# Optimization experiments

Hardware: AMD Instinct MI355X
Metric: run time of the kernel (lower is better)

Reference implementation:

```python
import jax, jax.numpy as jnp
import numpy as np

# Norse LIFParameters defaults (method='super', alpha=100)
DT = 1e-3
TAU_SYN_INV = 200.0   # 1 / 5e-3
TAU_MEM_INV = 100.0   # 1 / 1e-2
V_TH = 1.0
V_LEAK = 0.0
V_RESET = 0.0
ALPHA = 100.0

@jax.custom_vjp
def superspike(x):
    return (x > 0).astype(x.dtype)

def _ss_fwd(x):
    return superspike(x), x

def _ss_bwd(x, g):
    return (g / (ALPHA * jnp.abs(x) + 1.0) ** 2,)

superspike.defvjp(_ss_fwd, _ss_bwd)

T, B, F, H1, OUT = 100, 512, 784, 1024, 10

def setup_inputs() -> dict:
    key = jax.random.key(0)
    k1, k2, k3 = jax.random.split(key, 3)
    x = jax.random.normal(k1, (T, B, F), jnp.float32)
    # fc0: Linear(784, h1) with bias
    W0 = jax.random.normal(k2, (H1, F), jnp.float32) / np.sqrt(F)
    b0 = jnp.zeros((H1,), jnp.float32)
    # LILinearCell input_weights: Linear(h1, 10) without bias
    Wout = jax.random.normal(k3, (OUT, H1), jnp.float32) / np.sqrt(H1)
    return {"x": x, "W0": W0, "b0": b0, "Wout": Wout}

def reference(x, W0, b0, Wout):
    Tn, Bn, Fn = x.shape
    H = W0.shape[0]
    O = Wout.shape[0]

    def step(state, xt):
        v_lif, i_lif, v_li, i_li = state
        z_in = xt @ W0.T + b0                                    # [B, H]
        # LIF cell step
        v_dec = v_lif + DT * TAU_MEM_INV * ((V_LEAK - v_lif) + i_lif)
        i_dec = i_lif * (1.0 - DT * TAU_SYN_INV)
        z = superspike(v_dec - V_TH)                             # spikes [B, H]
        v_new = (1.0 - z) * v_dec + z * V_RESET
        i_new = i_dec + z_in
        # LI linear cell step (voltage output)
        v_li_new = v_li + DT * TAU_MEM_INV * ((V_LEAK - v_li) + i_li)
        i_li_new = i_li * (1.0 - DT * TAU_SYN_INV) + z @ Wout.T  # [B, O]
        return (v_new, i_new, v_li_new, i_li_new), v_li_new

    z0 = lambda s: jnp.zeros(s, x.dtype)
    init = (z0((Bn, H)), z0((Bn, H)), z0((Bn, O)), z0((Bn, O)))
    _, voltages = jax.lax.scan(step, init, x)
    return voltages  # [T, B, 10]
```

## Files before the change

kernel.cpp:

```cpp
#include <hip/hip_runtime.h>

#define T_TOT 100
#define BATCH 512
#define FIN   784
#define HID   1024
#define NOUT  10
#define KP    800
#define BK    32
#define KSTEPS 25
#define NGRP  16

typedef _Float16 f16x8 __attribute__((ext_vector_type(8)));
typedef float    f32x4 __attribute__((ext_vector_type(4)));

#define AS1C(p) ((const __attribute__((address_space(1))) void*)(p))
#define AS3(p)  ((__attribute__((address_space(3))) void*)(p))

__global__ __launch_bounds__(256)
void cvt_split(const float* __restrict__ src, _Float16* __restrict__ hi,
               _Float16* __restrict__ lo, int nrows)
{
    int idx = blockIdx.x * 256 + threadIdx.x;
    if (idx >= nrows * 100) return;
    int row = idx / 100;
    int k0  = (idx - row * 100) * 8;
    f16x8 h, l;
    if (k0 < FIN) {
        float4 a = *(const float4*)(src + (size_t)row * FIN + k0);
        float4 b = *(const float4*)(src + (size_t)row * FIN + k0 + 4);
        float xs[8] = {a.x, a.y, a.z, a.w, b.x, b.y, b.z, b.w};
        #pragma unroll
        for (int j = 0; j < 8; ++j) {
            _Float16 hh = (_Float16)xs[j];
            h[j] = hh;
            l[j] = (_Float16)((xs[j] - (float)hh) * 4096.0f);
        }
    } else {
        #pragma unroll
        for (int j = 0; j < 8; ++j) { h[j] = (_Float16)0.f; l[j] = (_Float16)0.f; }
    }
    *(f16x8*)(hi + (size_t)row * KP + k0) = h;
    *(f16x8*)(lo + (size_t)row * KP + k0) = l;
}

__global__ __launch_bounds__(256, 2)
void gemm_mfma(const _Float16* __restrict__ Xhi, const _Float16* __restrict__ Xlo,
               const _Float16* __restrict__ Whi, const _Float16* __restrict__ Wlo,
               const float* __restrict__ bias, float* __restrict__ Z, int mb)
{
    __shared__ char smem[65536];
    const int tid  = threadIdx.x;
    const int lane = tid & 63;
    const int wid  = tid >> 6;
    const int wm   = wid >> 1;
    const int wn   = wid & 1;
    const int fr   = lane & 15;
    const int fg   = lane >> 4;

    const int j = blockIdx.x;
    int bm, bn;
    if ((mb & 7) == 0) {
        bm = (j & 7) | ((j >> 6) << 3);
        bn = (j >> 3) & 7;
    } else {
        bm = j >> 3;
        bn = j & 7;
    }
    const size_t row0 = (size_t)bm * 128;
    const int    col0 = bn * 128;

    f32x4 accm[4][4], accc[4][4];
    #pragma unroll
    for (int a = 0; a < 4; ++a)
        #pragma unroll
        for (int b = 0; b < 4; ++b) {
            accm[a][b] = (f32x4){0.f, 0.f, 0.f, 0.f};
            accc[a][b] = (f32x4){0.f, 0.f, 0.f, 0.f};
        }

    auto stage = [&](int buf, int kt) {
        const int kof = kt * BK;
        #pragma unroll
        for (int q = 0; q < 2; ++q) {
            const int lin = q * 256 + tid;
            const int row = lin >> 2;
            const int pos = lin & 3;
            const int gg  = pos ^ ((row >> 1) & 3);
            const int ldsw = buf * 32768 + q * 4096 + wid * 1024;
            const size_t ga = (row0 + row) * (size_t)KP + kof + gg * 8;
            const size_t gb = (size_t)(col0 + row) * KP + kof + gg * 8;
            __builtin_amdgcn_global_load_lds(AS1C(Xhi + ga), AS3(smem + ldsw),         16, 0, 0);
            __builtin_amdgcn_global_load_lds(AS1C(Xlo + ga), AS3(smem + ldsw +  8192), 16, 0, 0);
            __builtin_amdgcn_global_load_lds(AS1C(Whi + gb), AS3(smem + ldsw + 16384), 16, 0, 0);
            __builtin_amdgcn_global_load_lds(AS1C(Wlo + gb), AS3(smem + ldsw + 24576), 16, 0, 0);
        }
    };

    auto compute = [&](int buf) {
        const char* base = smem + buf * 32768;
        f16x8 ah[4], al[4], bh[4], bl[4];
        #pragma unroll
        for (int mf = 0; mf < 4; ++mf) {
            const int row = wm * 64 + mf * 16 + fr;
            const int off = row * 64 + ((fg ^ ((row >> 1) & 3)) << 4);
            ah[mf] = *(const f16x8*)(base + off);
            al[mf] = *(const f16x8*)(base + 8192 + off);
        }
        #pragma unroll
        for (int nf = 0; nf < 4; ++nf) {
            const int row = wn * 64 + nf * 16 + fr;
            const int off = row * 64 + ((fg ^ ((row >> 1) & 3)) << 4);
            bh[nf] = *(const f16x8*)(base + 16384 + off);
            bl[nf] = *(const f16x8*)(base + 24576 + off);
        }
        #pragma unroll
        for (int mf = 0; mf < 4; ++mf)
            #pragma unroll
            for (int nf = 0; nf < 4; ++nf) {
                accm[mf][nf] = __builtin_amdgcn_mfma_f32_16x16x32_f16(ah[mf], bh[nf], accm[mf][nf], 0, 0, 0);
                accc[mf][nf] = __builtin_amdgcn_mfma_f32_16x16x32_f16(ah[mf], bl[nf], accc[mf][nf], 0, 0, 0);
                accc[mf][nf] = __builtin_amdgcn_mfma_f32_16x16x32_f16(al[mf], bh[nf], accc[mf][nf], 0, 0, 0);
            }
    };

    stage(0, 0);
    int buf = 0;
    for (int kt = 0; kt < KSTEPS; ++kt) {
        __syncthreads();
        if (kt + 1 < KSTEPS) stage(buf ^ 1, kt + 1);
        compute(buf);
        buf ^= 1;
    }

    #pragma unroll
    for (int nf = 0; nf < 4; ++nf) {
        const int colg = col0 + wn * 64 + nf * 16 + fr;
        const float bv = bias[colg];
        #pragma unroll
        for (int mf = 0; mf < 4; ++mf) {
            const size_t rowg = row0 + wm * 64 + mf * 16 + fg * 4;
            #pragma unroll
            for (int i = 0; i < 4; ++i)
                Z[(rowg + i) * HID + colg] =
                    accm[mf][nf][i] + accc[mf][nf][i] * 2.44140625e-4f + bv;
        }
    }
}

__device__ __forceinline__ float dpp_sum16(float v)
{
    int x;
    x = __builtin_amdgcn_update_dpp(0, __builtin_bit_cast(int, v), 0xB1, 0xF, 0xF, true);
    v += __builtin_bit_cast(float, x);
    x = __builtin_amdgcn_update_dpp(0, __builtin_bit_cast(int, v), 0x4E, 0xF, 0xF, true);
    v += __builtin_bit_cast(float, x);
    x = __builtin_amdgcn_update_dpp(0, __builtin_bit_cast(int, v), 0x141, 0xF, 0xF, true);
    v += __builtin_bit_cast(float, x);
    x = __builtin_amdgcn_update_dpp(0, __builtin_bit_cast(int, v), 0x140, 0xF, 0xF, true);
    v += __builtin_bit_cast(float, x);
    return v;
}

__global__ __launch_bounds__(256, 2)
void lif_scan(const float* __restrict__ Z, const float* __restrict__ Wout,
              float* __restrict__ S,
              float* __restrict__ st_v, float* __restrict__ st_i,
              int tn, int first, int last)
{
#pragma clang fp contract(off)
    const int tid   = threadIdx.x;
    const int b     = blockIdx.x;
    const int lane  = tid & 63;
    const int w     = tid >> 6;
    const int hglob = w * 256 + lane * 4;

    float wreg[NOUT][4];
    #pragma unroll
    for (int o = 0; o < NOUT; ++o) {
        float4 t4 = *(const float4*)&Wout[o * HID + hglob];
        wreg[o][0] = t4.x; wreg[o][1] = t4.y; wreg[o][2] = t4.z; wreg[o][3] = t4.w;
    }

    float v[4], cu[4];
    if (first) {
        #pragma unroll
        for (int jj = 0; jj < 4; ++jj) { v[jj] = 0.f; cu[jj] = 0.f; }
    } else {
        float4 tv = *(const float4*)&st_v[(size_t)b * HID + hglob];
        float4 ti = *(const float4*)&st_i[(size_t)b * HID + hglob];
        v[0]=tv.x; v[1]=tv.y; v[2]=tv.z; v[3]=tv.w;
        cu[0]=ti.x; cu[1]=ti.y; cu[2]=ti.z; cu[3]=ti.w;
    }

    const float* Zb = Z + (size_t)b * HID + hglob;
    float4 z0 = *(const float4*)Zb;
    float4 z1 = (tn > 1) ? *(const float4*)(Zb + (size_t)BATCH * HID)     : z0;
    float4 z2 = (tn > 2) ? *(const float4*)(Zb + (size_t)2 * BATCH * HID) : z1;

    const int g = w * 4 + (lane >> 4);

    for (int t = 0; t < tn; ++t) {
        float4 zc = z0; z0 = z1; z1 = z2;
        if (t + 3 < tn) z2 = *(const float4*)(Zb + (size_t)(t + 3) * BATCH * HID);

        const float za[4] = {zc.x, zc.y, zc.z, zc.w};
        float zf[4];
        bool anyz = false;
        #pragma unroll
        for (int jj = 0; jj < 4; ++jj) {
            float tmp  = (0.0f - v[jj]) + cu[jj];
            float vdec = v[jj] + 0.1f * tmp;
            bool  z    = vdec > 1.0f;
            zf[jj] = z ? 1.0f : 0.0f;
            anyz   = anyz || z;
            v[jj]  = z ? 0.0f : vdec;
            cu[jj] = cu[jj] * 0.8f + za[jj];
        }

        float p[NOUT];
        #pragma unroll
        for (int o = 0; o < NOUT; ++o) p[o] = 0.f;

        if (__any(anyz)) {
            if (anyz) {
                #pragma unroll
                for (int o = 0; o < NOUT; ++o)
                    p[o] = zf[0]*wreg[o][0] + zf[1]*wreg[o][1]
                         + zf[2]*wreg[o][2] + zf[3]*wreg[o][3];
            }
            #pragma unroll
            for (int o = 0; o < NOUT; ++o) p[o] = dpp_sum16(p[o]);
        }

        if ((lane & 15) == 0) {
            float* sp = S + ((size_t)t * BATCH + b) * (NGRP * NOUT) + g * NOUT;
            #pragma unroll
            for (int o = 0; o < NOUT; ++o) sp[o] = p[o];
        }
    }

    if (!last) {
        *(float4*)&st_v[(size_t)b * HID + hglob] = make_float4(v[0], v[1], v[2], v[3]);
        *(float4*)&st_i[(size_t)b * HID + hglob] = make_float4(cu[0], cu[1], cu[2], cu[3]);
    }
}

__global__ __launch_bounds__(256)
void li_scan(const float* __restrict__ S, float* __restrict__ out,
             float* __restrict__ st_vli, float* __restrict__ st_ili,
             int t0, int tn, int first, int last)
{
#pragma clang fp contract(off)
    const int id = blockIdx.x * 256 + threadIdx.x;
    if (id >= BATCH * NOUT) return;
    const int b = id / NOUT;
    const int o = id - b * NOUT;

    float vli = 0.f, ili = 0.f;
    if (!first) { vli = st_vli[id]; ili = st_ili[id]; }

    const float* Sp = S + (size_t)b * (NGRP * NOUT) + o;
    for (int t = 0; t < tn; ++t) {
        const float* p = Sp + (size_t)t * BATCH * (NGRP * NOUT);
        float s = 0.f;
        #pragma unroll
        for (int gg = 0; gg < NGRP; ++gg) s += p[gg * NOUT];
        float tmp  = (0.0f - vli) + ili;
        float vnew = vli + 0.1f * tmp;
        ili = ili * 0.8f + s;
        vli = vnew;
        out[((size_t)(t0 + t) * BATCH + b) * NOUT + o] = vnew;
    }
    if (!last) { st_vli[id] = vli; st_ili[id] = ili; }
}

extern "C" void kernel_launch(void* const* d_in, const int* in_sizes, int n_in,
                              void* d_out, int out_size, void* d_ws, size_t ws_size,
                              hipStream_t stream)
{
    const float* x    = (const float*)d_in[0];
    const float* W0   = (const float*)d_in[1];
    const float* b0   = (const float*)d_in[2];
    const float* Wout = (const float*)d_in[3];
    float* out = (float*)d_out;

    char* ws = (char*)d_ws;
    float* st_v   = (float*)ws;
    float* st_i   = st_v   + (size_t)BATCH * HID;
    float* st_vli = st_i   + (size_t)BATCH * HID;
    float* st_ili = st_vli + BATCH * NOUT;
    _Float16* Whi = (_Float16*)(st_ili + BATCH * NOUT);
    _Float16* Wlo = Whi + (size_t)HID * KP;
    char* dyn = (char*)(Wlo + (size_t)HID * KP);

    const size_t fixed = (size_t)(dyn - ws);
    const size_t per_t = (size_t)BATCH * HID * 4
                       + (size_t)BATCH * KP * 2 * 2
                       + (size_t)BATCH * NGRP * NOUT * 4;
    size_t avail = (ws_size > fixed) ? ws_size - fixed : 0;
    int tch = (int)(avail / per_t);
    if (tch > T_TOT) tch = T_TOT;
    if (tch >= 2) tch &= ~1;
    if (tch < 1) tch = 1;

    float*    Zbuf = (float*)dyn;
    _Float16* Xhi  = (_Float16*)(dyn + (size_t)tch * BATCH * HID * 4);
    _Float16* Xlo  = Xhi + (size_t)tch * BATCH * KP;
    float*    Sbuf = (float*)(Xlo + (size_t)tch * BATCH * KP);

    hipLaunchKernelGGL(cvt_split, dim3((HID * 100 + 255) / 256), dim3(256), 0, stream,
                       W0, Whi, Wlo, HID);

    for (int t0 = 0; t0 < T_TOT; t0 += tch) {
        const int tn    = (T_TOT - t0 < tch) ? (T_TOT - t0) : tch;
        const int nrows = tn * BATCH;
        const int mb    = nrows / 128;

        hipLaunchKernelGGL(cvt_split, dim3((nrows * 100 + 255) / 256), dim3(256), 0, stream,
                           x + (size_t)t0 * BATCH * FIN, Xhi, Xlo, nrows);
        hipLaunchKernelGGL(gemm_mfma, dim3(mb * 8), dim3(256), 0, stream,
                           Xhi, Xlo, Whi, Wlo, b0, Zbuf, mb);
        hipLaunchKernelGGL(lif_scan, dim3(BATCH), dim3(256), 0, stream,
                           Zbuf, Wout, Sbuf, st_v, st_i,
                           tn, (t0 == 0) ? 1 : 0, (t0 + tn >= T_TOT) ? 1 : 0);
        hipLaunchKernelGGL(li_scan, dim3((BATCH * NOUT + 255) / 256), dim3(256), 0, stream,
                           Sbuf, out, st_vli, st_ili,
                           t0, tn, (t0 == 0) ? 1 : 0, (t0 + tn >= T_TOT) ? 1 : 0);
    }
}
```

Baseline: 525.7 us.

## Split GEMM k-loop into hi/lo phases with partial waits; deepen LIF prefetch ring

The GEMM main loop now stages the hi and lo fp16 halves separately. It uses explicit vmcnt waits and raw barriers, so the hi-part MFMAs can start while the lo tiles are still loading, and the next hi tile is issued before current compute begins. MFMA sections are wrapped in s_setprio. The LIF scan kernel replaces its 3-deep Z prefetch with an 8-entry unrolled register ring to hide more global-load latency. This adds register pressure and relies on exact vmcnt counts to stay correct.

```diff
diff --git a/kernel.cpp b/kernel.cpp
--- a/kernel.cpp
+++ b/kernel.cpp
@@ -78,7 +78,7 @@
             accc[a][b] = (f32x4){0.f, 0.f, 0.f, 0.f};
         }
 
-    auto stage = [&](int buf, int kt) {
+    auto stage_hi = [&](int buf, int kt) {
         const int kof = kt * BK;
         #pragma unroll
         for (int q = 0; q < 2; ++q) {
@@ -90,46 +90,85 @@
             const size_t ga = (row0 + row) * (size_t)KP + kof + gg * 8;
             const size_t gb = (size_t)(col0 + row) * KP + kof + gg * 8;
             __builtin_amdgcn_global_load_lds(AS1C(Xhi + ga), AS3(smem + ldsw),         16, 0, 0);
+            __builtin_amdgcn_global_load_lds(AS1C(Whi + gb), AS3(smem + ldsw + 16384), 16, 0, 0);
+        }
+    };
+    auto stage_lo = [&](int buf, int kt) {
+        const int kof = kt * BK;
+        #pragma unroll
+        for (int q = 0; q < 2; ++q) {
+            const int lin = q * 256 + tid;
+            const int row = lin >> 2;
+            const int pos = lin & 3;
+            const int gg  = pos ^ ((row >> 1) & 3);
+            const int ldsw = buf * 32768 + q * 4096 + wid * 1024;
+            const size_t ga = (row0 + row) * (size_t)KP + kof + gg * 8;
+            const size_t gb = (size_t)(col0 + row) * KP + kof + gg * 8;
             __builtin_amdgcn_global_load_lds(AS1C(Xlo + ga), AS3(smem + ldsw +  8192), 16, 0, 0);
-            __builtin_amdgcn_global_load_lds(AS1C(Whi + gb), AS3(smem + ldsw + 16384), 16, 0, 0);
             __builtin_amdgcn_global_load_lds(AS1C(Wlo + gb), AS3(smem + ldsw + 24576), 16, 0, 0);
         }
     };
 
-    auto compute = [&](int buf) {
+    stage_hi(0, 0);
+    stage_lo(0, 0);
+
+    for (int kt = 0; kt < KSTEPS; ++kt) {
+        const int buf = kt & 1;
         const char* base = smem + buf * 32768;
         f16x8 ah[4], al[4], bh[4], bl[4];
+
+        asm volatile("s_waitcnt vmcnt(4)" ::: "memory");
+        __builtin_amdgcn_s_barrier();
+        asm volatile("" ::: "memory");
+        if (kt + 1 < KSTEPS) stage_hi(buf ^ 1, kt + 1);
+
         #pragma unroll
         for (int mf = 0; mf < 4; ++mf) {
             const int row = wm * 64 + mf * 16 + fr;
             const int off = row * 64 + ((fg ^ ((row >> 1) & 3)) << 4);
             ah[mf] = *(const f16x8*)(base + off);
-            al[mf] = *(const f16x8*)(base + 8192 + off);
         }
         #pragma unroll
         for (int nf = 0; nf < 4; ++nf) {
             const int row = wn * 64 + nf * 16 + fr;
             const int off = row * 64 + ((fg ^ ((row >> 1) & 3)) << 4);
             bh[nf] = *(const f16x8*)(base + 16384 + off);
+        }
+        __builtin_amdgcn_s_setprio(1);
+        #pragma unroll
+        for (int mf = 0; mf < 4; ++mf)
+            #pragma unroll
+            for (int nf = 0; nf < 4; ++nf)
+                accm[mf][nf] = __builtin_amdgcn_mfma_f32_16x16x32_f16(ah[mf], bh[nf], accm[mf][nf], 0, 0, 0);
+        __builtin_amdgcn_s_setprio(0);
+
+        if (kt + 1 < KSTEPS) asm volatile("s_waitcnt vmcnt(4)" ::: "memory");
+        else                 asm volatile("s_waitcnt vmcnt(0)" ::: "memory");
+        __builtin_amdgcn_s_barrier();
+        asm volatile("" ::: "memory");
+        if (kt + 1 < KSTEPS) stage_lo(buf ^ 1, kt + 1);
+
+        #pragma unroll
+        for (int mf = 0; mf < 4; ++mf) {
+            const int row = wm * 64 + mf * 16 + fr;
+            const int off = row * 64 + ((fg ^ ((row >> 1) & 3)) << 4);
+            al[mf] = *(const f16x8*)(base + 8192 + off);
+        }
+        #pragma unroll
+        for (int nf = 0; nf < 4; ++nf) {
+            const int row = wn * 64 + nf * 16 + fr;
+            const int off = row * 64 + ((fg ^ ((row >> 1) & 3)) << 4);
             bl[nf] = *(const f16x8*)(base + 24576 + off);
         }
+        __builtin_amdgcn_s_setprio(1);
         #pragma unroll
         for (int mf = 0; mf < 4; ++mf)
             #pragma unroll
             for (int nf = 0; nf < 4; ++nf) {
-                accm[mf][nf] = __builtin_amdgcn_mfma_f32_16x16x32_f16(ah[mf], bh[nf], accm[mf][nf], 0, 0, 0);
                 accc[mf][nf] = __builtin_amdgcn_mfma_f32_16x16x32_f16(ah[mf], bl[nf], accc[mf][nf], 0, 0, 0);
                 accc[mf][nf] = __builtin_amdgcn_mfma_f32_16x16x32_f16(al[mf], bh[nf], accc[mf][nf], 0, 0, 0);
             }
-    };
-
-    stage(0, 0);
-    int buf = 0;
-    for (int kt = 0; kt < KSTEPS; ++kt) {
-        __syncthreads();
-        if (kt + 1 < KSTEPS) stage(buf ^ 1, kt + 1);
-        compute(buf);
-        buf ^= 1;
+        __builtin_amdgcn_s_setprio(0);
     }
 
     #pragma unroll
@@ -192,50 +231,59 @@
         cu[0]=ti.x; cu[1]=ti.y; cu[2]=ti.z; cu[3]=ti.w;
     }
 
-    const float* Zb = Z + (size_t)b * HID + hglob;
-    float4 z0 = *(const float4*)Zb;
-    float4 z1 = (tn > 1) ? *(const float4*)(Zb + (size_t)BATCH * HID)     : z0;
-    float4 z2 = (tn > 2) ? *(const float4*)(Zb + (size_t)2 * BATCH * HID) : z1;
-
-    const int g = w * 4 + (lane >> 4);
-
-    for (int t = 0; t < tn; ++t) {
-        float4 zc = z0; z0 = z1; z1 = z2;
-        if (t + 3 < tn) z2 = *(const float4*)(Zb + (size_t)(t + 3) * BATCH * HID);
-
-        const float za[4] = {zc.x, zc.y, zc.z, zc.w};
-        float zf[4];
-        bool anyz = false;
-        #pragma unroll
-        for (int jj = 0; jj < 4; ++jj) {
-            float tmp  = (0.0f - v[jj]) + cu[jj];
-            float vdec = v[jj] + 0.1f * tmp;
-            bool  z    = vdec > 1.0f;
-            zf[jj] = z ? 1.0f : 0.0f;
-            anyz   = anyz || z;
-            v[jj]  = z ? 0.0f : vdec;
-            cu[jj] = cu[jj] * 0.8f + za[jj];
-        }
-
-        float p[NOUT];
-        #pragma unroll
-        for (int o = 0; o < NOUT; ++o) p[o] = 0.f;
-
-        if (__any(anyz)) {
-            if (anyz) {
+    const float*  Zb    = Z + (size_t)b * HID + hglob;
+    const size_t  ZSTEP = (size_t)BATCH * HID;
+    const int     g     = w * 4 + (lane >> 4);
+
+    float4 ring[8];
+    #pragma unroll
+    for (int u = 0; u < 8; ++u)
+        ring[u] = (u < tn) ? *(const float4*)(Zb + (size_t)u * ZSTEP)
+                           : make_float4(0.f, 0.f, 0.f, 0.f);
+
+    for (int tb = 0; tb < tn; tb += 8) {
+        #pragma unroll
+        for (int u = 0; u < 8; ++u) {
+            const int t = tb + u;
+            if (t >= tn) break;
+            float4 zc = ring[u];
+            if (t + 8 < tn)
+                ring[u] = *(const float4*)(Zb + (size_t)(t + 8) * ZSTEP);
+
+            const float za[4] = {zc.x, zc.y, zc.z, zc.w};
+            float zf[4];
+            bool anyz = false;
+            #pragma unroll
+            for (int jj = 0; jj < 4; ++jj) {
+                float tmp  = (0.0f - v[jj]) + cu[jj];
+                float vdec = v[jj] + 0.1f * tmp;
+                bool  z    = vdec > 1.0f;
+                zf[jj] = z ? 1.0f : 0.0f;
+                anyz   = anyz || z;
+                v[jj]  = z ? 0.0f : vdec;
+                cu[jj] = cu[jj] * 0.8f + za[jj];
+            }
+
+            float p[NOUT];
+            #pragma unroll
+            for (int o = 0; o < NOUT; ++o) p[o] = 0.f;
+
+            if (__any(anyz)) {
+                if (anyz) {
+                    #pragma unroll
+                    for (int o = 0; o < NOUT; ++o)
+                        p[o] = zf[0]*wreg[o][0] + zf[1]*wreg[o][1]
+                             + zf[2]*wreg[o][2] + zf[3]*wreg[o][3];
+                }
                 #pragma unroll
-                for (int o = 0; o < NOUT; ++o)
-                    p[o] = zf[0]*wreg[o][0] + zf[1]*wreg[o][1]
-                         + zf[2]*wreg[o][2] + zf[3]*wreg[o][3];
+                for (int o = 0; o < NOUT; ++o) p[o] = dpp_sum16(p[o]);
             }
-            #pragma unroll
-            for (int o = 0; o < NOUT; ++o) p[o] = dpp_sum16(p[o]);
-        }
-
-        if ((lane & 15) == 0) {
-            float* sp = S + ((size_t)t * BATCH + b) * (NGRP * NOUT) + g * NOUT;
-            #pragma unroll
-            for (int o = 0; o < NOUT; ++o) sp[o] = p[o];
+
+            if ((lane & 15) == 0) {
+                float* sp = S + ((size_t)t * BATCH + b) * (NGRP * NOUT) + g * NOUT;
+                #pragma unroll
+                for (int o = 0; o < NOUT; ++o) sp[o] = p[o];
+            }
         }
     }
 
```

After: 484.7 us. -7.8%, faster.

## Fuse fp32-to-fp16 hi/lo split of X into GEMM and deepen scan prefetch

Applied to the files above, without the earlier changes.

The GEMM now loads fp32 X straight from global memory into registers, splits it into fp16 hi/lo parts and writes them to LDS inside the k-loop. This removes the separate X conversion pass and its workspace round trip, and frees that workspace so larger time chunks fit. The LIF scan prefetches Z eight steps ahead through a register ring. The LI scan assigns 16 lanes per output and reduces the group partials with a DPP sum, prefetching four steps ahead. The trade-off is more register pressure and conversion ALU work inside the GEMM, and the X load is no longer asynchronous.

```diff
diff --git a/kernel.cpp b/kernel.cpp
--- a/kernel.cpp
+++ b/kernel.cpp
@@ -10,6 +10,11 @@
 #define KSTEPS 25
 #define NGRP  16
 
+#define A_HI 0
+#define A_LO 8192
+#define B_HI 16384
+#define B_LO 24576
+
 typedef _Float16 f16x8 __attribute__((ext_vector_type(8)));
 typedef float    f32x4 __attribute__((ext_vector_type(4)));
 
@@ -44,9 +49,9 @@
 }
 
 __global__ __launch_bounds__(256, 2)
-void gemm_mfma(const _Float16* __restrict__ Xhi, const _Float16* __restrict__ Xlo,
-               const _Float16* __restrict__ Whi, const _Float16* __restrict__ Wlo,
-               const float* __restrict__ bias, float* __restrict__ Z, int mb)
+void gemm_fused(const float* __restrict__ X,
+                const _Float16* __restrict__ Whi, const _Float16* __restrict__ Wlo,
+                const float* __restrict__ bias, float* __restrict__ Z, int mb)
 {
     __shared__ char smem[65536];
     const int tid  = threadIdx.x;
@@ -78,7 +83,39 @@
             accc[a][b] = (f32x4){0.f, 0.f, 0.f, 0.f};
         }
 
-    auto stage = [&](int buf, int kt) {
+    const int arow  = tid >> 1;
+    const int ahalf = tid & 1;
+    float4 ar[4];
+    auto aload = [&](int kt) {
+        const int kof = kt * BK + ahalf * 16;
+        const float* src = X + (row0 + arow) * (size_t)FIN + kof;
+        #pragma unroll
+        for (int c = 0; c < 4; ++c)
+            ar[c] = (kof + c * 4 < FIN) ? *(const float4*)(src + c * 4)
+                                        : make_float4(0.f, 0.f, 0.f, 0.f);
+    };
+    auto cvtwrite = [&](int buf) {
+        char* base = smem + buf * 32768;
+        #pragma unroll
+        for (int cc = 0; cc < 2; ++cc) {
+            float xs[8];
+            *(float4*)&xs[0] = ar[cc * 2];
+            *(float4*)&xs[4] = ar[cc * 2 + 1];
+            f16x8 h, l;
+            #pragma unroll
+            for (int e = 0; e < 8; ++e) {
+                _Float16 hh = (_Float16)xs[e];
+                h[e] = hh;
+                l[e] = (_Float16)((xs[e] - (float)hh) * 4096.0f);
+            }
+            const int ch  = ahalf * 2 + cc;
+            const int chs = ch ^ ((arow >> 1) & 3);
+            const int off = arow * 64 + chs * 16;
+            *(f16x8*)(base + A_HI + off) = h;
+            *(f16x8*)(base + A_LO + off) = l;
+        }
+    };
+    auto stageB = [&](int buf, int kt) {
         const int kof = kt * BK;
         #pragma unroll
         for (int q = 0; q < 2; ++q) {
@@ -87,12 +124,9 @@
             const int pos = lin & 3;
             const int gg  = pos ^ ((row >> 1) & 3);
             const int ldsw = buf * 32768 + q * 4096 + wid * 1024;
-            const size_t ga = (row0 + row) * (size_t)KP + kof + gg * 8;
             const size_t gb = (size_t)(col0 + row) * KP + kof + gg * 8;
-            __builtin_amdgcn_global_load_lds(AS1C(Xhi + ga), AS3(smem + ldsw),         16, 0, 0);
-            __builtin_amdgcn_global_load_lds(AS1C(Xlo + ga), AS3(smem + ldsw +  8192), 16, 0, 0);
-            __builtin_amdgcn_global_load_lds(AS1C(Whi + gb), AS3(smem + ldsw + 16384), 16, 0, 0);
-            __builtin_amdgcn_global_load_lds(AS1C(Wlo + gb), AS3(smem + ldsw + 24576), 16, 0, 0);
+            __builtin_amdgcn_global_load_lds(AS1C(Whi + gb), AS3(smem + ldsw + B_HI), 16, 0, 0);
+            __builtin_amdgcn_global_load_lds(AS1C(Wlo + gb), AS3(smem + ldsw + B_LO), 16, 0, 0);
         }
     };
 
@@ -103,15 +137,15 @@
         for (int mf = 0; mf < 4; ++mf) {
             const int row = wm * 64 + mf * 16 + fr;
             const int off = row * 64 + ((fg ^ ((row >> 1) & 3)) << 4);
-            ah[mf] = *(const f16x8*)(base + off);
-            al[mf] = *(const f16x8*)(base + 8192 + off);
+            ah[mf] = *(const f16x8*)(base + A_HI + off);
+            al[mf] = *(const f16x8*)(base + A_LO + off);
         }
         #pragma unroll
         for (int nf = 0; nf < 4; ++nf) {
             const int row = wn * 64 + nf * 16 + fr;
             const int off = row * 64 + ((fg ^ ((row >> 1) & 3)) << 4);
-            bh[nf] = *(const f16x8*)(base + 16384 + off);
-            bl[nf] = *(const f16x8*)(base + 24576 + off);
+            bh[nf] = *(const f16x8*)(base + B_HI + off);
+            bl[nf] = *(const f16x8*)(base + B_LO + off);
         }
         #pragma unroll
         for (int mf = 0; mf < 4; ++mf)
@@ -123,12 +157,19 @@
             }
     };
 
-    stage(0, 0);
+    aload(0);
+    stageB(0, 0);
+    cvtwrite(0);
+
     int buf = 0;
     for (int kt = 0; kt < KSTEPS; ++kt) {
         __syncthreads();
-        if (kt + 1 < KSTEPS) stage(buf ^ 1, kt + 1);
+        if (kt + 1 < KSTEPS) {
+            aload(kt + 1);
+            stageB(buf ^ 1, kt + 1);
+        }
         compute(buf);
+        if (kt + 1 < KSTEPS) cvtwrite(buf ^ 1);
         buf ^= 1;
     }
 
@@ -192,50 +233,59 @@
         cu[0]=ti.x; cu[1]=ti.y; cu[2]=ti.z; cu[3]=ti.w;
     }
 
-    const float* Zb = Z + (size_t)b * HID + hglob;
-    float4 z0 = *(const float4*)Zb;
-    float4 z1 = (tn > 1) ? *(const float4*)(Zb + (size_t)BATCH * HID)     : z0;
-    float4 z2 = (tn > 2) ? *(const float4*)(Zb + (size_t)2 * BATCH * HID) : z1;
-
-    const int g = w * 4 + (lane >> 4);
-
-    for (int t = 0; t < tn; ++t) {
-        float4 zc = z0; z0 = z1; z1 = z2;
-        if (t + 3 < tn) z2 = *(const float4*)(Zb + (size_t)(t + 3) * BATCH * HID);
-
-        const float za[4] = {zc.x, zc.y, zc.z, zc.w};
-        float zf[4];
-        bool anyz = false;
-        #pragma unroll
-        for (int jj = 0; jj < 4; ++jj) {
-            float tmp  = (0.0f - v[jj]) + cu[jj];
-            float vdec = v[jj] + 0.1f * tmp;
-            bool  z    = vdec > 1.0f;
-            zf[jj] = z ? 1.0f : 0.0f;
-            anyz   = anyz || z;
-            v[jj]  = z ? 0.0f : vdec;
-            cu[jj] = cu[jj] * 0.8f + za[jj];
-        }
-
-        float p[NOUT];
-        #pragma unroll
-        for (int o = 0; o < NOUT; ++o) p[o] = 0.f;
-
-        if (__any(anyz)) {
-            if (anyz) {
+    const float*  Zb    = Z + (size_t)b * HID + hglob;
+    const size_t  ZSTEP = (size_t)BATCH * HID;
+    const int     g     = w * 4 + (lane >> 4);
+
+    float4 ring[8];
+    #pragma unroll
+    for (int u = 0; u < 8; ++u)
+        ring[u] = (u < tn) ? *(const float4*)(Zb + (size_t)u * ZSTEP)
+                           : make_float4(0.f, 0.f, 0.f, 0.f);
+
+    for (int tb = 0; tb < tn; tb += 8) {
+        #pragma unroll
+        for (int u = 0; u < 8; ++u) {
+            const int t = tb + u;
+            if (t >= tn) break;
+            float4 zc = ring[u];
+            if (t + 8 < tn)
+                ring[u] = *(const float4*)(Zb + (size_t)(t + 8) * ZSTEP);
+
+            const float za[4] = {zc.x, zc.y, zc.z, zc.w};
+            float zf[4];
+            bool anyz = false;
+            #pragma unroll
+            for (int jj = 0; jj < 4; ++jj) {
+                float tmp  = (0.0f - v[jj]) + cu[jj];
+                float vdec = v[jj] + 0.1f * tmp;
+                bool  z    = vdec > 1.0f;
+                zf[jj] = z ? 1.0f : 0.0f;
+                anyz   = anyz || z;
+                v[jj]  = z ? 0.0f : vdec;
+                cu[jj] = cu[jj] * 0.8f + za[jj];
+            }
+
+            float p[NOUT];
+            #pragma unroll
+            for (int o = 0; o < NOUT; ++o) p[o] = 0.f;
+
+            if (__any(anyz)) {
+                if (anyz) {
+                    #pragma unroll
+                    for (int o = 0; o < NOUT; ++o)
+                        p[o] = zf[0]*wreg[o][0] + zf[1]*wreg[o][1]
+                             + zf[2]*wreg[o][2] + zf[3]*wreg[o][3];
+                }
                 #pragma unroll
-                for (int o = 0; o < NOUT; ++o)
-                    p[o] = zf[0]*wreg[o][0] + zf[1]*wreg[o][1]
-                         + zf[2]*wreg[o][2] + zf[3]*wreg[o][3];
-            }
-            #pragma unroll
-            for (int o = 0; o < NOUT; ++o) p[o] = dpp_sum16(p[o]);
-        }
-
-        if ((lane & 15) == 0) {
-            float* sp = S + ((size_t)t * BATCH + b) * (NGRP * NOUT) + g * NOUT;
-            #pragma unroll
-            for (int o = 0; o < NOUT; ++o) sp[o] = p[o];
+                for (int o = 0; o < NOUT; ++o) p[o] = dpp_sum16(p[o]);
+            }
+
+            if ((lane & 15) == 0) {
+                float* sp = S + ((size_t)t * BATCH + b) * (NGRP * NOUT) + g * NOUT;
+                #pragma unroll
+                for (int o = 0; o < NOUT; ++o) sp[o] = p[o];
+            }
         }
     }
 
@@ -251,27 +301,39 @@
              int t0, int tn, int first, int last)
 {
 #pragma clang fp contract(off)
-    const int id = blockIdx.x * 256 + threadIdx.x;
-    if (id >= BATCH * NOUT) return;
-    const int b = id / NOUT;
-    const int o = id - b * NOUT;
+    const int team = blockIdx.x * 16 + (threadIdx.x >> 4);
+    const int g    = threadIdx.x & 15;
+    const int b    = team / NOUT;
+    const int o    = team - b * NOUT;
 
     float vli = 0.f, ili = 0.f;
-    if (!first) { vli = st_vli[id]; ili = st_ili[id]; }
-
-    const float* Sp = S + (size_t)b * (NGRP * NOUT) + o;
-    for (int t = 0; t < tn; ++t) {
-        const float* p = Sp + (size_t)t * BATCH * (NGRP * NOUT);
-        float s = 0.f;
-        #pragma unroll
-        for (int gg = 0; gg < NGRP; ++gg) s += p[gg * NOUT];
-        float tmp  = (0.0f - vli) + ili;
-        float vnew = vli + 0.1f * tmp;
-        ili = ili * 0.8f + s;
-        vli = vnew;
-        out[((size_t)(t0 + t) * BATCH + b) * NOUT + o] = vnew;
-    }
-    if (!last) { st_vli[id] = vli; st_ili[id] = ili; }
+    if (!first) { vli = st_vli[team]; ili = st_ili[team]; }
+
+    const float* Sp   = S + ((size_t)b * NGRP + g) * NOUT + o;
+    const size_t STEP = (size_t)BATCH * NGRP * NOUT;
+
+    float rg[4];
+    #pragma unroll
+    for (int u = 0; u < 4; ++u)
+        rg[u] = (u < tn) ? Sp[(size_t)u * STEP] : 0.f;
+
+    for (int tb = 0; tb < tn; tb += 4) {
+        #pragma unroll
+        for (int u = 0; u < 4; ++u) {
+            const int t = tb + u;
+            if (t >= tn) break;
+            float val = rg[u];
+            if (t + 4 < tn) rg[u] = Sp[(size_t)(t + 4) * STEP];
+            float s = dpp_sum16(val);
+            float tmp  = (0.0f - vli) + ili;
+            float vnew = vli + 0.1f * tmp;
+            ili = ili * 0.8f + s;
+            vli = vnew;
+            if (g == 0)
+                out[((size_t)(t0 + t) * BATCH + b) * NOUT + o] = vnew;
+        }
+    }
+    if (!last && g == 0) { st_vli[team] = vli; st_ili[team] = ili; }
 }
 
 extern "C" void kernel_launch(void* const* d_in, const int* in_sizes, int n_in,
@@ -295,7 +357,6 @@
 
     const size_t fixed = (size_t)(dyn - ws);
     const size_t per_t = (size_t)BATCH * HID * 4
-                       + (size_t)BATCH * KP * 2 * 2
                        + (size_t)BATCH * NGRP * NOUT * 4;
     size_t avail = (ws_size > fixed) ? ws_size - fixed : 0;
     int tch = (int)(avail / per_t);
@@ -303,10 +364,8 @@
     if (tch >= 2) tch &= ~1;
     if (tch < 1) tch = 1;
 
-    float*    Zbuf = (float*)dyn;
-    _Float16* Xhi  = (_Float16*)(dyn + (size_t)tch * BATCH * HID * 4);
-    _Float16* Xlo  = Xhi + (size_t)tch * BATCH * KP;
-    float*    Sbuf = (float*)(Xlo + (size_t)tch * BATCH * KP);
+    float* Zbuf = (float*)dyn;
+    float* Sbuf = (float*)(dyn + (size_t)tch * BATCH * HID * 4);
 
     hipLaunchKernelGGL(cvt_split, dim3((HID * 100 + 255) / 256), dim3(256), 0, stream,
                        W0, Whi, Wlo, HID);
@@ -316,14 +375,12 @@
         const int nrows = tn * BATCH;
         const int mb    = nrows / 128;
 
-        hipLaunchKernelGGL(cvt_split, dim3((nrows * 100 + 255) / 256), dim3(256), 0, stream,
-                           x + (size_t)t0 * BATCH * FIN, Xhi, Xlo, nrows);
-        hipLaunchKernelGGL(gemm_mfma, dim3(mb * 8), dim3(256), 0, stream,
-                           Xhi, Xlo, Whi, Wlo, b0, Zbuf, mb);
+        hipLaunchKernelGGL(gemm_fused, dim3(mb * 8), dim3(256), 0, stream,
+                           x + (size_t)t0 * BATCH * FIN, Whi, Wlo, b0, Zbuf, mb);
         hipLaunchKernelGGL(lif_scan, dim3(BATCH), dim3(256), 0, stream,
                            Zbuf, Wout, Sbuf, st_v, st_i,
                            tn, (t0 == 0) ? 1 : 0, (t0 + tn >= T_TOT) ? 1 : 0);
-        hipLaunchKernelGGL(li_scan, dim3((BATCH * NOUT + 255) / 256), dim3(256), 0, stream,
+        hipLaunchKernelGGL(li_scan, dim3((BATCH * NOUT) / 16), dim3(256), 0, stream,
                            Sbuf, out, st_vli, st_ili,
                            t0, tn, (t0 == 0) ? 1 : 0, (t0 + tn >= T_TOT) ? 1 : 0);
     }
```

Measured after the change: 450.3 us. 1.17x faster.
